# Kernel tuning notes

Hardware: AMD Instinct MI355X
Metric: run time of the kernel (lower is better)

The kernel has to match this reference:

```python
import jax, jax.numpy as jnp
import numpy as np

# Crossbar analog-compute constants (match init_kwargs)
R_HRS = 1.0e6      # high-resistance state (ohms)
R_LRS = 1.0e4      # low-resistance state (ohms)
RP = 2.0           # parasitic wire resistance per segment (ohms)
BITS = 4           # conductance quantization bits
TS = 512           # max_array_size (tile size)
G_MIN = 1.0 / R_HRS
G_MAX = 1.0 / R_LRS


def weight_mapping(w):
    """Linearly map a weight tile to conductances in [G_MIN, G_MAX].
    Returns (cond, scale s, w_min) so the mapping can be inverted."""
    wmin = w.min()
    wmax = w.max()
    s = (G_MAX - G_MIN) / (wmax - wmin + 1e-12)
    cond = (w - wmin) * s + G_MIN
    return cond, s, wmin


def quantization(cond):
    """Quantize conductances to 2**BITS uniform levels in [G_MIN, G_MAX]."""
    n_levels = 2 ** BITS - 1
    step = (G_MAX - G_MIN) / n_levels
    return jnp.round((cond - G_MIN) / step) * step + G_MIN


def jeong_model(cond, x):
    """Nonlinear analog IV model: series parasitic wire resistance added per
    device position (Jeong-style approximation). cond: [ts_in, ts_out],
    x: [B, ts_in] -> currents [B, ts_out]."""
    ts_in, ts_out = cond.shape
    i = jnp.arange(ts_in, dtype=cond.dtype)[:, None]
    j = jnp.arange(ts_out, dtype=cond.dtype)[None, :]
    r_wire = RP * ((ts_in - i) + (j + 1.0))
    g_eff = 1.0 / (1.0 / cond + r_wire)
    return x @ g_eff


def ideal_model(cond, x):
    return x @ cond


def process_tile(w_tile, x_tile):
    """One crossbar tile: map -> quantize -> nonlinear IV -> correction -> unmap.
    w_tile: [TS, TS], x_tile: [B, TS] -> partial output [B, TS]."""
    cond, s, wmin = weight_mapping(w_tile)
    cond = quantization(cond)                      # bits>0 and non-ideal model
    currents = jeong_model(cond, x_tile)           # [B, TS]
    ideal = ideal_model(cond, x_tile)              # [B, TS]
    # correction: rescale nonlinear currents to the ideal dynamic range
    coeff = (ideal.max(axis=1) - ideal.min(axis=1)) / (
        currents.max(axis=1) - currents.min(axis=1) + 1e-8)
    currents = (currents - currents.mean(axis=1, keepdims=True)) * coeff[:, None] \
        + ideal.mean(axis=1, keepdims=True)
    # output_unmapping: invert cond = (w - wmin)*s + G_MIN given I = x @ cond
    offset = x_tile.sum(axis=1, keepdims=True) * (G_MIN - s * wmin)
    return (currents - offset) / s


def setup_inputs() -> dict:
    key = jax.random.key(0)
    kx, kw, kb = jax.random.split(key, 3)
    x = jax.random.normal(kx, (1024, 4096), dtype=jnp.float32)
    weight = jax.random.normal(kw, (4096, 4096), dtype=jnp.float32) * 0.05
    bias = jax.random.normal(kb, (4096,), dtype=jnp.float32) * 0.01
    return {"x": x, "weight": weight, "bias": bias}


def reference(x, weight, bias):
    B, in_features = x.shape
    _, out_features = weight.shape
    it, ot = in_features // TS, out_features // TS
    # weight tiles: [it, ot, TS, TS]; x tiles: [it, B, TS]
    w_tiles = weight.reshape(it, TS, ot, TS).transpose(0, 2, 1, 3)
    x_tiles = x.reshape(B, it, TS).transpose(1, 0, 2)
    tile_fn = jax.vmap(jax.vmap(process_tile, in_axes=(0, None)),  # over ot
                       in_axes=(0, 0))                             # over it
    parts = tile_fn(w_tiles, x_tiles)          # [it, ot, B, TS]
    out = parts.sum(axis=0)                    # [ot, B, TS]
    out = out.transpose(1, 0, 2).reshape(B, out_features)
    return out + bias
```

## Files before the change

### kernel.cpp

```cpp
#include <hip/hip_runtime.h>
#include <hip/hip_fp16.h>
#include <cstdint>

#define DI __device__ __forceinline__

typedef _Float16 f16;
typedef _Float16 half8 __attribute__((ext_vector_type(8)));
typedef float f32x4 __attribute__((ext_vector_type(4)));

constexpr int NF  = 4096;
constexpr int TSZ = 512;

constexpr float G_MIN  = (float)(1.0 / 1.0e6);
constexpr float GRANGE = (float)(1.0e-4 - 1.0e-6);
constexpr float QSTEP  = (float)((1.0e-4 - 1.0e-6) / 15.0);

__global__ void convert_x(const float* __restrict__ x, f16* __restrict__ xh) {
    int idx = blockIdx.x * 256 + threadIdx.x;
    float4 v = ((const float4*)x)[idx];
    union { f16 h[4]; uint2 u; } o;
    o.h[0] = (f16)v.x; o.h[1] = (f16)v.y; o.h[2] = (f16)v.z; o.h[3] = (f16)v.w;
    ((uint2*)xh)[idx] = o.u;
}

__global__ __launch_bounds__(256)
void tile_minmax1(const float* __restrict__ w,
                  float* __restrict__ pmin, float* __restrict__ pmax) {
    int bid = blockIdx.x;
    int tile = bid >> 4, sub = bid & 15;
    int it = tile >> 3, jt = tile & 7;
    const float* base = w + (size_t)(it * TSZ + sub * 32) * NF + jt * TSZ;
    float mn = 3.4e38f, mx = -3.4e38f;
    int t = threadIdx.x;
#pragma unroll
    for (int i = 0; i < 16; ++i) {
        int idx = i * 256 + t;
        int r = idx >> 7, c4 = idx & 127;
        float4 v = ((const float4*)(base + (size_t)r * NF))[c4];
        mn = fminf(mn, fminf(fminf(v.x, v.y), fminf(v.z, v.w)));
        mx = fmaxf(mx, fmaxf(fmaxf(v.x, v.y), fmaxf(v.z, v.w)));
    }
    for (int d = 1; d < 64; d <<= 1) {
        mn = fminf(mn, __shfl_xor(mn, d)); mx = fmaxf(mx, __shfl_xor(mx, d));
    }
    __shared__ float smn[4], smx[4];
    int wv = t >> 6;
    if ((t & 63) == 0) { smn[wv] = mn; smx[wv] = mx; }
    __syncthreads();
    if (t == 0) {
        pmin[bid] = fminf(fminf(smn[0], smn[1]), fminf(smn[2], smn[3]));
        pmax[bid] = fmaxf(fmaxf(smx[0], smx[1]), fmaxf(smx[2], smx[3]));
    }
}

__global__ __launch_bounds__(1024)
void tile_minmax2(const float* __restrict__ pmin, const float* __restrict__ pmax,
                  float* __restrict__ wmin, float* __restrict__ wmax) {
    int t = threadIdx.x;
    float mn = pmin[t], mx = pmax[t];
#pragma unroll
    for (int d = 1; d < 16; d <<= 1) {
        mn = fminf(mn, __shfl_xor(mn, d));
        mx = fmaxf(mx, __shfl_xor(mx, d));
    }
    if ((t & 15) == 0) { wmin[t >> 4] = mn; wmax[t >> 4] = mx; }
}

__global__ void transform_w(const float* __restrict__ w,
                            const float* __restrict__ wmin_, const float* __restrict__ wmax_,
                            f16* __restrict__ wq_t, f16* __restrict__ h_t) {
#pragma clang fp contract(off)
    __shared__ f16 lwq[64][72];
    __shared__ f16 lh[64][72];
    int tile = blockIdx.x >> 6; int it = tile >> 3, jt = tile & 7;
    int sub = blockIdx.x & 63; int k0 = (sub >> 3) << 6, n0 = (sub & 7) << 6;
    float wmin = wmin_[tile], wmax = wmax_[tile];
    float s = GRANGE / (wmax - wmin + 1e-12f);
    float inv_s = 1.0f / s;
    int t = threadIdx.x, cn = t & 63, r0 = t >> 6;
    for (int rr = 0; rr < 16; ++rr) {
        int rk = rr * 4 + r0;
        float wv = w[(size_t)(it * TSZ + k0 + rk) * NF + jt * TSZ + n0 + cn];
        float cond  = (wv - wmin) * s + G_MIN;
        float q     = rintf((cond - G_MIN) / QSTEP);
        float condq = q * QSTEP + G_MIN;
        float wqv   = (condq - G_MIN) * inv_s + wmin;
        float rw    = 2.0f * ((512.0f - (float)(k0 + rk)) + ((float)(n0 + cn) + 1.0f));
        float ge    = 1.0f / (1.0f / condq + rw);
        lwq[rk][cn] = (f16)wqv;
        lh[rk][cn]  = (f16)(ge * inv_s);
    }
    __syncthreads();
    for (int pp = 0; pp < 8; ++pp) {
        int nl = pp * 8 + (t >> 5);
        int kp = (t & 31) * 2;
        union { f16 h[2]; uint32_t u; } a, b;
        a.h[0] = lwq[kp][nl]; a.h[1] = lwq[kp + 1][nl];
        b.h[0] = lh[kp][nl];  b.h[1] = lh[kp + 1][nl];
        size_t obase = (size_t)tile * TSZ * TSZ + (size_t)(n0 + nl) * TSZ + k0 + kp;
        *(uint32_t*)(wq_t + obase) = a.u;
        *(uint32_t*)(h_t + obase)  = b.u;
    }
}

DI void gl16(const void* g, void* l) {
    auto gp = reinterpret_cast<const uint32_t __attribute__((address_space(1)))*>(
        reinterpret_cast<uintptr_t>(g));
    auto lp = reinterpret_cast<uint32_t __attribute__((address_space(3)))*>(
        reinterpret_cast<uintptr_t>(l));
    __builtin_amdgcn_global_load_lds(gp, lp, 16, 0, 0);
}

template <int MODE>
__global__ __launch_bounds__(256, 2)
void gemm_tile(const f16* __restrict__ A, const f16* __restrict__ Bmat,
               f16* __restrict__ Cout, float* __restrict__ pmx,
               float* __restrict__ pmn, float* __restrict__ psm) {
    __shared__ __align__(16) f16 As[2][4096];
    __shared__ __align__(16) f16 Bs[2][4096];
    __shared__ float sred[128][2][4];

    int bx = blockIdx.x;
    int tile = bx >> 5, mb = (bx >> 2) & 7, nb = bx & 3;
    int it = tile >> 3;
    int t = threadIdx.x, lane = t & 63, w = t >> 6;
    int wr = w >> 1, wc = w & 1;

    const f16* Ab = A + (size_t)(mb * 128) * NF + it * TSZ;
    const f16* Bb = Bmat + ((size_t)tile * TSZ + nb * 128) * TSZ;

    int l1 = t, l2 = t + 256;
    int r1 = l1 >> 2, k1 = ((l1 & 3) ^ ((r1 >> 1) & 3)) * 8;
    int r2 = l2 >> 2, k2 = ((l2 & 3) ^ ((r2 >> 1) & 3)) * 8;
    const f16* a1 = Ab + (size_t)r1 * NF + k1;
    const f16* a2 = Ab + (size_t)r2 * NF + k2;
    const f16* b1 = Bb + (size_t)r1 * TSZ + k1;
    const f16* b2 = Bb + (size_t)r2 * TSZ + k2;

    f32x4 acc[4][4] = {};

    gl16(a1, &As[0][w * 512]); gl16(a2, &As[0][2048 + w * 512]);
    gl16(b1, &Bs[0][w * 512]); gl16(b2, &Bs[0][2048 + w * 512]);
    a1 += 32; a2 += 32; b1 += 32; b2 += 32;
    __syncthreads();

    int rA = wr * 64 + (lane & 15);
    int rB = wc * 64 + (lane & 15);
    int sl = lane >> 4;

    for (int kt = 0; kt < 16; ++kt) {
        int cur = kt & 1, nxt = cur ^ 1;
        if (kt < 15) {
            gl16(a1, &As[nxt][w * 512]); gl16(a2, &As[nxt][2048 + w * 512]);
            gl16(b1, &Bs[nxt][w * 512]); gl16(b2, &Bs[nxt][2048 + w * 512]);
            a1 += 32; a2 += 32; b1 += 32; b2 += 32;
        }
        half8 af[4], bf[4];
#pragma unroll
        for (int m = 0; m < 4; ++m) {
            int row = rA + m * 16;
            af[m] = *(const half8*)&As[cur][row * 32 + ((sl ^ ((row >> 1) & 3)) << 3)];
        }
#pragma unroll
        for (int n = 0; n < 4; ++n) {
            int row = rB + n * 16;
            bf[n] = *(const half8*)&Bs[cur][row * 32 + ((sl ^ ((row >> 1) & 3)) << 3)];
        }
#pragma unroll
        for (int m = 0; m < 4; ++m)
#pragma unroll
            for (int n = 0; n < 4; ++n)
                acc[m][n] = __builtin_amdgcn_mfma_f32_16x16x32_f16(af[m], bf[n], acc[m][n], 0, 0, 0);
        __syncthreads();
    }

#pragma unroll
    for (int m = 0; m < 4; ++m) {
#pragma unroll
        for (int r = 0; r < 4; ++r) {
            float mx = -3.4e38f, mn = 3.4e38f, sm = 0.f;
#pragma unroll
            for (int n = 0; n < 4; ++n) {
                float v = acc[m][n][r];
                mx = fmaxf(mx, v); mn = fminf(mn, v); sm += v;
            }
#pragma unroll
            for (int d = 1; d < 16; d <<= 1) {
                mx = fmaxf(mx, __shfl_xor(mx, d));
                mn = fminf(mn, __shfl_xor(mn, d));
                sm += __shfl_xor(sm, d);
            }
            if ((lane & 15) == 0) {
                int row = wr * 64 + m * 16 + (lane >> 4) * 4 + r;
                sred[row][wc][0] = mx; sred[row][wc][1] = mn; sred[row][wc][2] = sm;
            }
        }
    }
    __syncthreads();
    if (t < 128) {
        float mx = fmaxf(sred[t][0][0], sred[t][1][0]);
        float mn = fminf(sred[t][0][1], sred[t][1][1]);
        float sm = sred[t][0][2] + sred[t][1][2];
        size_t idx = ((size_t)tile * 1024 + mb * 128 + t) * 4 + nb;
        pmx[idx] = mx; pmn[idx] = mn; psm[idx] = sm;
    }

    if (MODE == 1) {
        size_t base = ((size_t)tile * 1024 + mb * 128) * 512 + nb * 128;
#pragma unroll
        for (int m = 0; m < 4; ++m) {
            int row0 = wr * 64 + m * 16 + (lane >> 4) * 4;
#pragma unroll
            for (int n = 0; n < 4; ++n) {
                int col = wc * 64 + n * 16 + (lane & 15);
#pragma unroll
                for (int r = 0; r < 4; ++r)
                    Cout[base + (size_t)(row0 + r) * 512 + col] = (f16)acc[m][n][r];
            }
        }
    }
}

__global__ void alphabeta(const float* __restrict__ pmx, const float* __restrict__ pmn,
                          const float* __restrict__ psm,
                          const float* __restrict__ qmx, const float* __restrict__ qmn,
                          const float* __restrict__ qsm,
                          const float* __restrict__ wmin_, const float* __restrict__ wmax_,
                          float* __restrict__ alpha, float* __restrict__ beta) {
    int i = blockIdx.x * 256 + threadIdx.x;
    int tile = i >> 10;
    float s = GRANGE / (wmax_[tile] - wmin_[tile] + 1e-12f);
    size_t p = (size_t)i * 4;
    float pmax = fmaxf(fmaxf(pmx[p], pmx[p+1]), fmaxf(pmx[p+2], pmx[p+3]));
    float pmin = fminf(fminf(pmn[p], pmn[p+1]), fminf(pmn[p+2], pmn[p+3]));
    float psum = psm[p] + psm[p+1] + psm[p+2] + psm[p+3];
    float qmax = fmaxf(fmaxf(qmx[p], qmx[p+1]), fmaxf(qmx[p+2], qmx[p+3]));
    float qmin = fminf(fminf(qmn[p], qmn[p+1]), fminf(qmn[p+2], qmn[p+3]));
    float qsum = qsm[p] + qsm[p+1] + qsm[p+2] + qsm[p+3];
    float coeff = (s * (pmax - pmin)) / (s * (qmax - qmin) + 1e-8f);
    float meanP = psum * (1.0f / 512.0f);
    float meanQ = qsum * (1.0f / 512.0f);
    alpha[i] = coeff;
    beta[i]  = meanP - coeff * meanQ;
}

__global__ __launch_bounds__(256)
void combine(const f16* __restrict__ Q,
             const float* __restrict__ alpha, const float* __restrict__ beta,
             const float* __restrict__ bias, float* __restrict__ out) {
    int bid = blockIdx.x;
    int jt = bid & 7, b = bid >> 3;
    int t = threadIdx.x;
    float o0 = 0.f, o1 = 0.f, bsum = 0.f;
#pragma unroll
    for (int i = 0; i < 8; ++i) {
        int tile = i * 8 + jt;
        int ab = tile * 1024 + b;
        float a = alpha[ab];
        bsum += beta[ab];
        union { uint32_t u; f16 h[2]; } q2;
        q2.u = ((const uint32_t*)(Q + ((size_t)tile * 1024 + b) * 512))[t];
        o0 = fmaf(a, (float)q2.h[0], o0);
        o1 = fmaf(a, (float)q2.h[1], o1);
    }
    float2 bv = ((const float2*)(bias + jt * 512))[t];
    float2 ov; ov.x = o0 + bsum + bv.x; ov.y = o1 + bsum + bv.y;
    ((float2*)(out + (size_t)b * 4096))[jt * 256 + t] = ov;
}

extern "C" void kernel_launch(void* const* d_in, const int* in_sizes, int n_in,
                              void* d_out, int out_size, void* d_ws, size_t ws_size,
                              hipStream_t stream) {
    const float* x    = (const float*)d_in[0];
    const float* wt   = (const float*)d_in[1];
    const float* bias = (const float*)d_in[2];
    float* out = (float*)d_out;
    char* ws = (char*)d_ws;

    float* wmin = (float*)ws;
    float* wmax = (float*)(ws + 256);
    float* pmin1 = (float*)(ws + 512);
    float* pmax1 = (float*)(ws + 512 + 4096);
    size_t off = 512 + 8192;
    f16* xh   = (f16*)(ws + off); off += (size_t)1024 * 4096 * 2;
    f16* wq_t = (f16*)(ws + off); off += (size_t)4096 * 4096 * 2;
    f16* h_t  = (f16*)(ws + off); off += (size_t)4096 * 4096 * 2;
    float* pmx = (float*)(ws + off); off += (size_t)64 * 1024 * 4 * 4;
    float* pmn = (float*)(ws + off); off += (size_t)64 * 1024 * 4 * 4;
    float* psm = (float*)(ws + off); off += (size_t)64 * 1024 * 4 * 4;
    float* qmx = (float*)(ws + off); off += (size_t)64 * 1024 * 4 * 4;
    float* qmn = (float*)(ws + off); off += (size_t)64 * 1024 * 4 * 4;
    float* qsm = (float*)(ws + off); off += (size_t)64 * 1024 * 4 * 4;
    float* alpha = (float*)(ws + off); off += (size_t)64 * 1024 * 4;
    float* beta  = (float*)(ws + off); off += (size_t)64 * 1024 * 4;
    f16* Q    = (f16*)(ws + off);

    convert_x   <<<4096, 256,  0, stream>>>(x, xh);
    tile_minmax1<<<1024, 256,  0, stream>>>(wt, pmin1, pmax1);
    tile_minmax2<<<1,    1024, 0, stream>>>(pmin1, pmax1, wmin, wmax);
    transform_w <<<4096, 256,  0, stream>>>(wt, wmin, wmax, wq_t, h_t);
    gemm_tile<0><<<2048, 256,  0, stream>>>(xh, wq_t, nullptr, pmx, pmn, psm);
    gemm_tile<1><<<2048, 256,  0, stream>>>(xh, h_t, Q, qmx, qmn, qsm);
    alphabeta   <<<256,  256,  0, stream>>>(pmx, pmn, psm, qmx, qmn, qsm,
                                            wmin, wmax, alpha, beta);
    combine     <<<8192, 256,  0, stream>>>(Q, alpha, beta, bias, out);
}
```

Baseline: 292.7 us.

## Fuse the two crossbar GEMMs into one kernel sharing A tiles

Replaces two separate GEMM launches (quantized conductance and effective conductance) with one kernel that loads each activation tile once and computes both products with two accumulator sets. This removes the duplicate global/LDS traffic for A and one kernel launch. In exchange, register and LDS usage per block roughly double for accumulators and B buffers, which risks spills or lower occupancy.

```diff
diff --git a/kernel.cpp b/kernel.cpp
--- a/kernel.cpp
+++ b/kernel.cpp
@@ -111,13 +111,14 @@
     __builtin_amdgcn_global_load_lds(gp, lp, 16, 0, 0);
 }
 
-template <int MODE>
 __global__ __launch_bounds__(256, 2)
-void gemm_tile(const f16* __restrict__ A, const f16* __restrict__ Bmat,
-               f16* __restrict__ Cout, float* __restrict__ pmx,
-               float* __restrict__ pmn, float* __restrict__ psm) {
+void gemm_fused(const f16* __restrict__ A, const f16* __restrict__ B1,
+                const f16* __restrict__ B2, f16* __restrict__ Qout,
+                float* __restrict__ pmx, float* __restrict__ pmn, float* __restrict__ psm,
+                float* __restrict__ qmx, float* __restrict__ qmn, float* __restrict__ qsm) {
     __shared__ __align__(16) f16 As[2][4096];
-    __shared__ __align__(16) f16 Bs[2][4096];
+    __shared__ __align__(16) f16 B1s[2][4096];
+    __shared__ __align__(16) f16 B2s[2][4096];
     __shared__ float sred[128][2][4];
 
     int bx = blockIdx.x;
@@ -126,22 +127,27 @@
     int t = threadIdx.x, lane = t & 63, w = t >> 6;
     int wr = w >> 1, wc = w & 1;
 
-    const f16* Ab = A + (size_t)(mb * 128) * NF + it * TSZ;
-    const f16* Bb = Bmat + ((size_t)tile * TSZ + nb * 128) * TSZ;
+    const f16* Ab  = A  + (size_t)(mb * 128) * NF + it * TSZ;
+    const f16* B1b = B1 + ((size_t)tile * TSZ + nb * 128) * TSZ;
+    const f16* B2b = B2 + ((size_t)tile * TSZ + nb * 128) * TSZ;
 
     int l1 = t, l2 = t + 256;
     int r1 = l1 >> 2, k1 = ((l1 & 3) ^ ((r1 >> 1) & 3)) * 8;
     int r2 = l2 >> 2, k2 = ((l2 & 3) ^ ((r2 >> 1) & 3)) * 8;
-    const f16* a1 = Ab + (size_t)r1 * NF + k1;
-    const f16* a2 = Ab + (size_t)r2 * NF + k2;
-    const f16* b1 = Bb + (size_t)r1 * TSZ + k1;
-    const f16* b2 = Bb + (size_t)r2 * TSZ + k2;
-
-    f32x4 acc[4][4] = {};
-
-    gl16(a1, &As[0][w * 512]); gl16(a2, &As[0][2048 + w * 512]);
-    gl16(b1, &Bs[0][w * 512]); gl16(b2, &Bs[0][2048 + w * 512]);
-    a1 += 32; a2 += 32; b1 += 32; b2 += 32;
+    const f16* a1  = Ab  + (size_t)r1 * NF  + k1;
+    const f16* a2  = Ab  + (size_t)r2 * NF  + k2;
+    const f16* b11 = B1b + (size_t)r1 * TSZ + k1;
+    const f16* b12 = B1b + (size_t)r2 * TSZ + k2;
+    const f16* b21 = B2b + (size_t)r1 * TSZ + k1;
+    const f16* b22 = B2b + (size_t)r2 * TSZ + k2;
+
+    f32x4 accP[4][4] = {};
+    f32x4 accQ[4][4] = {};
+
+    gl16(a1,  &As[0][w * 512]);  gl16(a2,  &As[0][2048 + w * 512]);
+    gl16(b11, &B1s[0][w * 512]); gl16(b12, &B1s[0][2048 + w * 512]);
+    gl16(b21, &B2s[0][w * 512]); gl16(b22, &B2s[0][2048 + w * 512]);
+    a1 += 32; a2 += 32; b11 += 32; b12 += 32; b21 += 32; b22 += 32;
     __syncthreads();
 
     int rA = wr * 64 + (lane & 15);
@@ -151,11 +157,12 @@
     for (int kt = 0; kt < 16; ++kt) {
         int cur = kt & 1, nxt = cur ^ 1;
         if (kt < 15) {
-            gl16(a1, &As[nxt][w * 512]); gl16(a2, &As[nxt][2048 + w * 512]);
-            gl16(b1, &Bs[nxt][w * 512]); gl16(b2, &Bs[nxt][2048 + w * 512]);
-            a1 += 32; a2 += 32; b1 += 32; b2 += 32;
+            gl16(a1,  &As[nxt][w * 512]);  gl16(a2,  &As[nxt][2048 + w * 512]);
+            gl16(b11, &B1s[nxt][w * 512]); gl16(b12, &B1s[nxt][2048 + w * 512]);
+            gl16(b21, &B2s[nxt][w * 512]); gl16(b22, &B2s[nxt][2048 + w * 512]);
+            a1 += 32; a2 += 32; b11 += 32; b12 += 32; b21 += 32; b22 += 32;
         }
-        half8 af[4], bf[4];
+        half8 af[4], bf1[4], bf2[4];
 #pragma unroll
         for (int m = 0; m < 4; ++m) {
             int row = rA + m * 16;
@@ -164,59 +171,70 @@
 #pragma unroll
         for (int n = 0; n < 4; ++n) {
             int row = rB + n * 16;
-            bf[n] = *(const half8*)&Bs[cur][row * 32 + ((sl ^ ((row >> 1) & 3)) << 3)];
+            int o = row * 32 + ((sl ^ ((row >> 1) & 3)) << 3);
+            bf1[n] = *(const half8*)&B1s[cur][o];
+            bf2[n] = *(const half8*)&B2s[cur][o];
         }
 #pragma unroll
         for (int m = 0; m < 4; ++m)
 #pragma unroll
-            for (int n = 0; n < 4; ++n)
-                acc[m][n] = __builtin_amdgcn_mfma_f32_16x16x32_f16(af[m], bf[n], acc[m][n], 0, 0, 0);
+            for (int n = 0; n < 4; ++n) {
+                accP[m][n] = __builtin_amdgcn_mfma_f32_16x16x32_f16(af[m], bf1[n], accP[m][n], 0, 0, 0);
+                accQ[m][n] = __builtin_amdgcn_mfma_f32_16x16x32_f16(af[m], bf2[n], accQ[m][n], 0, 0, 0);
+            }
         __syncthreads();
     }
 
+#define ROW_STATS(ACC, DMX, DMN, DSM)                                          \
+    {                                                                          \
+        _Pragma("unroll")                                                      \
+        for (int m = 0; m < 4; ++m) {                                          \
+            _Pragma("unroll")                                                  \
+            for (int r = 0; r < 4; ++r) {                                      \
+                float mx = -3.4e38f, mn = 3.4e38f, sm = 0.f;                   \
+                _Pragma("unroll")                                              \
+                for (int n = 0; n < 4; ++n) {                                  \
+                    float v = ACC[m][n][r];                                    \
+                    mx = fmaxf(mx, v); mn = fminf(mn, v); sm += v;             \
+                }                                                              \
+                _Pragma("unroll")                                              \
+                for (int d = 1; d < 16; d <<= 1) {                             \
+                    mx = fmaxf(mx, __shfl_xor(mx, d));                         \
+                    mn = fminf(mn, __shfl_xor(mn, d));                         \
+                    sm += __shfl_xor(sm, d);                                   \
+                }                                                              \
+                if ((lane & 15) == 0) {                                        \
+                    int row = wr * 64 + m * 16 + (lane >> 4) * 4 + r;          \
+                    sred[row][wc][0] = mx; sred[row][wc][1] = mn;              \
+                    sred[row][wc][2] = sm;                                     \
+                }                                                              \
+            }                                                                  \
+        }                                                                      \
+        __syncthreads();                                                       \
+        if (t < 128) {                                                         \
+            float mx = fmaxf(sred[t][0][0], sred[t][1][0]);                    \
+            float mn = fminf(sred[t][0][1], sred[t][1][1]);                    \
+            float sm = sred[t][0][2] + sred[t][1][2];                          \
+            size_t idx = ((size_t)tile * 1024 + mb * 128 + t) * 4 + nb;        \
+            DMX[idx] = mx; DMN[idx] = mn; DSM[idx] = sm;                       \
+        }                                                                      \
+        __syncthreads();                                                       \
+    }
+
+    ROW_STATS(accP, pmx, pmn, psm)
+    ROW_STATS(accQ, qmx, qmn, qsm)
+#undef ROW_STATS
+
+    size_t base = ((size_t)tile * 1024 + mb * 128) * 512 + nb * 128;
 #pragma unroll
     for (int m = 0; m < 4; ++m) {
-#pragma unroll
-        for (int r = 0; r < 4; ++r) {
-            float mx = -3.4e38f, mn = 3.4e38f, sm = 0.f;
-#pragma unroll
-            for (int n = 0; n < 4; ++n) {
-                float v = acc[m][n][r];
-                mx = fmaxf(mx, v); mn = fminf(mn, v); sm += v;
-            }
-#pragma unroll
-            for (int d = 1; d < 16; d <<= 1) {
-                mx = fmaxf(mx, __shfl_xor(mx, d));
-                mn = fminf(mn, __shfl_xor(mn, d));
-                sm += __shfl_xor(sm, d);
-            }
-            if ((lane & 15) == 0) {
-                int row = wr * 64 + m * 16 + (lane >> 4) * 4 + r;
-                sred[row][wc][0] = mx; sred[row][wc][1] = mn; sred[row][wc][2] = sm;
-            }
-        }
-    }
-    __syncthreads();
-    if (t < 128) {
-        float mx = fmaxf(sred[t][0][0], sred[t][1][0]);
-        float mn = fminf(sred[t][0][1], sred[t][1][1]);
-        float sm = sred[t][0][2] + sred[t][1][2];
-        size_t idx = ((size_t)tile * 1024 + mb * 128 + t) * 4 + nb;
-        pmx[idx] = mx; pmn[idx] = mn; psm[idx] = sm;
-    }
-
-    if (MODE == 1) {
-        size_t base = ((size_t)tile * 1024 + mb * 128) * 512 + nb * 128;
-#pragma unroll
-        for (int m = 0; m < 4; ++m) {
-            int row0 = wr * 64 + m * 16 + (lane >> 4) * 4;
-#pragma unroll
-            for (int n = 0; n < 4; ++n) {
-                int col = wc * 64 + n * 16 + (lane & 15);
-#pragma unroll
-                for (int r = 0; r < 4; ++r)
-                    Cout[base + (size_t)(row0 + r) * 512 + col] = (f16)acc[m][n][r];
-            }
+        int row0 = wr * 64 + m * 16 + (lane >> 4) * 4;
+#pragma unroll
+        for (int n = 0; n < 4; ++n) {
+            int col = wc * 64 + n * 16 + (lane & 15);
+#pragma unroll
+            for (int r = 0; r < 4; ++r)
+                Qout[base + (size_t)(row0 + r) * 512 + col] = (f16)accQ[m][n][r];
         }
     }
 }
@@ -299,8 +317,8 @@
     tile_minmax1<<<1024, 256,  0, stream>>>(wt, pmin1, pmax1);
     tile_minmax2<<<1,    1024, 0, stream>>>(pmin1, pmax1, wmin, wmax);
     transform_w <<<4096, 256,  0, stream>>>(wt, wmin, wmax, wq_t, h_t);
-    gemm_tile<0><<<2048, 256,  0, stream>>>(xh, wq_t, nullptr, pmx, pmn, psm);
-    gemm_tile<1><<<2048, 256,  0, stream>>>(xh, h_t, Q, qmx, qmn, qsm);
+    gemm_fused  <<<2048, 256,  0, stream>>>(xh, wq_t, h_t, Q,
+                                            pmx, pmn, psm, qmx, qmn, qsm);
     alphabeta   <<<256,  256,  0, stream>>>(pmx, pmn, psm, qmx, qmn, qsm,
                                             wmin, wmax, alpha, beta);
     combine     <<<8192, 256,  0, stream>>>(Q, alpha, beta, bias, out);
```

Result: faster. 285.6 us (-2.4%).
